# Performance work log

Measured on AMD Instinct MI355X. Metric: run time of the kernel, lower is better.

The kernel has to match this reference:

```python
import jax, jax.numpy as jnp
import numpy as np

DIM = 768
NUM_HEADS = 12
HEAD_DIM = DIM // NUM_HEADS
SCALE = HEAD_DIM ** -0.5


def setup_inputs() -> dict:
    key = jax.random.key(0)
    k1, k2, k3 = jax.random.split(key, 3)
    x = jax.random.normal(k1, (32, 577, DIM), dtype=jnp.float32)
    # torch nn.Linear weights are [out_features, in_features]
    W_qkv = jax.random.normal(k2, (3 * DIM, DIM), dtype=jnp.float32) * (DIM ** -0.5)
    W_proj = jax.random.normal(k3, (DIM, DIM), dtype=jnp.float32) * (DIM ** -0.5)
    b_proj = jnp.zeros((DIM,), dtype=jnp.float32)
    return {"x": x, "W_qkv": W_qkv, "W_proj": W_proj, "b_proj": b_proj}


def reference(x, W_qkv, W_proj, b_proj):
    B, N, C = x.shape
    H, D = NUM_HEADS, C // NUM_HEADS
    # qkv: [B, N, 3C] -> [3, B, H, N, D]
    qkv = (x @ W_qkv.T).reshape(B, N, 3, H, D).transpose(2, 0, 3, 1, 4)
    q, k, v = qkv[0], qkv[1], qkv[2]
    attn = jnp.einsum('bhnd,bhmd->bhnm', q, k) * SCALE
    attn = jax.nn.softmax(attn, axis=-1)
    out = jnp.einsum('bhnm,bhmd->bhnd', attn, v)  # [B, H, N, D]
    out = out.transpose(0, 2, 1, 3).reshape(B, N, C)
    return out @ W_proj.T + b_proj
```

## Files before the change

kernel.cpp:

```cpp
#include <hip/hip_runtime.h>
#include <math.h>

#define SEQ    577
#define BATCH  32
#define DIM    768
#define NHEAD  12
#define HDIM   64
#define MROWS  (BATCH * SEQ)
#define QKVN   (3 * DIM)

using half4   = __attribute__((ext_vector_type(4))) _Float16;
using half8   = __attribute__((ext_vector_type(8))) _Float16;
using floatx4 = __attribute__((ext_vector_type(4))) float;

typedef __attribute__((address_space(1))) const unsigned int GU;
typedef __attribute__((address_space(3))) unsigned int LU;

__device__ __forceinline__ void gld_lds16(const _Float16* g, _Float16* l) {
    __builtin_amdgcn_global_load_lds((const GU*)g, (LU*)l, 16, 0, 0);
}

__device__ __forceinline__ unsigned lds_addr(const void* p) {
    return (unsigned)(size_t)(LU*)p;
}

__global__ void cvt3_f32_f16(const float* __restrict__ a, _Float16* __restrict__ ao, int na4,
                             const float* __restrict__ b, _Float16* __restrict__ bo, int nb4,
                             const float* __restrict__ c, _Float16* __restrict__ co, int nc4)
{
    int i = blockIdx.x * blockDim.x + threadIdx.x;
    int stride = gridDim.x * blockDim.x;
    int total = na4 + nb4 + nc4;
    for (; i < total; i += stride) {
        const float4* src; half4* dst; int j = i;
        if (j < na4)            { src = (const float4*)a; dst = (half4*)ao; }
        else if ((j -= na4) < nb4) { src = (const float4*)b; dst = (half4*)bo; }
        else { j -= nb4;          src = (const float4*)c; dst = (half4*)co; }
        float4 v = src[j];
        half4 h;
        h[0] = (_Float16)v.x; h[1] = (_Float16)v.y;
        h[2] = (_Float16)v.z; h[3] = (_Float16)v.w;
        dst[j] = h;
    }
}

template<int OUT_HALF, int HAS_BIAS, int SCALEQ>
__global__ __launch_bounds__(256) void gemm_f16_lds(
    const _Float16* __restrict__ A, const _Float16* __restrict__ B,
    const float* __restrict__ bias, void* __restrict__ Cp,
    int M, int N, int K, int npm, int npn)
{
    __shared__ _Float16 As[2][128 * 32];
    __shared__ _Float16 Bs[2][128 * 32];

    const int GROUP = 8;
    int pid  = blockIdx.x;
    int ngrp = GROUP * npn;
    int g    = pid / ngrp;
    int fm   = g * GROUP;
    int gm   = npm - fm; if (gm > GROUP) gm = GROUP;
    int pm   = fm + (pid % ngrp) % gm;
    int pn   = (pid % ngrp) / gm;
    const int m0 = pm * 128, n0 = pn * 128;

    const int t    = threadIdx.x, lane = t & 63, wv = t >> 6;
    const int quad = lane >> 4,   ln   = lane & 15;
    const int wm   = wv >> 1,     wn   = wv & 1;

    floatx4 acc[4][4];
#pragma unroll
    for (int mt = 0; mt < 4; mt++)
#pragma unroll
        for (int nt = 0; nt < 4; nt++) acc[mt][nt] = {0.f, 0.f, 0.f, 0.f};

    const int sr  = wv * 32 + (lane >> 2);
    const int scl = (lane & 3) * 8;
    const int scg = ((lane & 3) ^ ((lane >> 3) & 3)) * 8;
    int ma0 = m0 + sr;      if (ma0 > M - 1) ma0 = M - 1;
    int ma1 = m0 + sr + 16; if (ma1 > M - 1) ma1 = M - 1;
    const _Float16* Ag0 = A + (size_t)ma0 * K + scg;
    const _Float16* Ag1 = A + (size_t)ma1 * K + scg;
    const _Float16* Bg0 = B + (size_t)(n0 + sr) * K + scg;
    const _Float16* Bg1 = B + (size_t)(n0 + sr + 16) * K + scg;
    const int l0 = sr * 32 + scl;
    const int l1 = (sr + 16) * 32 + scl;

    const int nk = K >> 5;

#define STAGE_G(it, buf)                                            \
    {                                                               \
        const int kn_ = (it) << 5;                                  \
        gld_lds16(Ag0 + kn_, &As[(buf)][l0]);                       \
        gld_lds16(Ag1 + kn_, &As[(buf)][l1]);                       \
        gld_lds16(Bg0 + kn_, &Bs[(buf)][l0]);                       \
        gld_lds16(Bg1 + kn_, &Bs[(buf)][l1]);                       \
    }

    STAGE_G(0, 0);
    STAGE_G(1, 1);

    const int rq = (ln >> 1) & 3;

    for (int it = 0; it < nk; it++) {
        const int cur = it & 1;

        if (it + 1 < nk) asm volatile("s_waitcnt vmcnt(4)" ::: "memory");
        else             asm volatile("s_waitcnt vmcnt(0)" ::: "memory");
        __builtin_amdgcn_s_barrier();
        __builtin_amdgcn_sched_barrier(0);

        half8 af[4], bf[4];
#pragma unroll
        for (int mt = 0; mt < 4; mt++)
            af[mt] = *(const half8*)&As[cur][(wm * 64 + mt * 16 + ln) * 32 + ((quad ^ rq) << 3)];
#pragma unroll
        for (int nt = 0; nt < 4; nt++)
            bf[nt] = *(const half8*)&Bs[cur][(wn * 64 + nt * 16 + ln) * 32 + ((quad ^ rq) << 3)];
#pragma unroll
        for (int mt = 0; mt < 4; mt++)
#pragma unroll
            for (int nt = 0; nt < 4; nt++)
                acc[mt][nt] = __builtin_amdgcn_mfma_f32_16x16x32_f16(
                    af[mt], bf[nt], acc[mt][nt], 0, 0, 0);

        __builtin_amdgcn_sched_barrier(0);
        __builtin_amdgcn_s_barrier();
        if (it + 2 < nk) STAGE_G(it + 2, cur);
    }
#undef STAGE_G

    float bv[4];
    if constexpr (HAS_BIAS) {
#pragma unroll
        for (int nt = 0; nt < 4; nt++) bv[nt] = bias[n0 + wn * 64 + nt * 16 + ln];
    }
    float*    C32 = (float*)Cp;
    _Float16* C16 = (_Float16*)Cp;
#pragma unroll
    for (int mt = 0; mt < 4; mt++)
#pragma unroll
        for (int r = 0; r < 4; r++) {
            int m = m0 + wm * 64 + mt * 16 + quad * 4 + r;
            if (m < M) {
#pragma unroll
                for (int nt = 0; nt < 4; nt++) {
                    int col = n0 + wn * 64 + nt * 16 + ln;
                    float v = acc[mt][nt][r];
                    if constexpr (HAS_BIAS) v += bv[nt];
                    if constexpr (SCALEQ) { if (col < DIM) v *= 0.18033688f; }
                    if constexpr (OUT_HALF) C16[(size_t)m * N + col] = (_Float16)v;
                    else                    C32[(size_t)m * N + col] = v;
                }
            }
        }
}

__global__ __launch_bounds__(256) void attn_f16(
    const _Float16* __restrict__ qkv, _Float16* __restrict__ outp)
{
    __shared__ _Float16 Ks[2][64 * 64];
    __shared__ _Float16 Vs[2][64 * 64];

    const int t    = threadIdx.x, lane = t & 63, wv = t >> 6;
    const int quad = lane >> 4,   ln   = lane & 15;
    const int q0   = blockIdx.x * 128;
    const int hd   = blockIdx.y,  b    = blockIdx.z;
    const _Float16* base = qkv + (size_t)b * SEQ * QKVN;

    half8 qreg[2][2];
#pragma unroll
    for (int qc = 0; qc < 2; qc++) {
        int q = q0 + wv * 32 + qc * 16 + ln; if (q >= SEQ) q = SEQ - 1;
#pragma unroll
        for (int kd = 0; kd < 2; kd++)
            qreg[qc][kd] = *(const half8*)(base + (size_t)q * QKVN + hd * HDIM + kd * 32 + quad * 8);
    }

    const int krow = t >> 3;
    const int kdc  = (t & 7) ^ (krow & 7);
    const int vkey = ((t >> 7) << 4) + (((t >> 3) & 3) << 2) + ((t >> 1) & 3);
    const int vd0  = (((t >> 5) & 3) << 4) + ((t & 1) << 3);
    const _Float16* kcst = base + DIM     + hd * HDIM + kdc * 8;
    const _Float16* vcst = base + 2 * DIM + hd * HDIM + vd0;

    float lr[2] = {0.f, 0.f};
    floatx4 o[2][4];
#pragma unroll
    for (int qc = 0; qc < 2; qc++)
#pragma unroll
        for (int dt = 0; dt < 4; dt++) o[qc][dt] = {0.f, 0.f, 0.f, 0.f};

    const unsigned vb0 = lds_addr(&Vs[0][0]) + lane * 8;

    gld_lds16(kcst + (size_t)krow * QKVN,        &Ks[0][t * 8]);
    gld_lds16(kcst + (size_t)(krow + 32) * QKVN, &Ks[0][(t + 256) * 8]);
    gld_lds16(vcst + (size_t)vkey * QKVN,        &Vs[0][t * 8]);
    gld_lds16(vcst + (size_t)(vkey + 32) * QKVN, &Vs[0][(t + 256) * 8]);

    for (int kt0 = 0; kt0 < 10; kt0++) {
        const int cur = kt0 & 1;
        const int k0  = kt0 * 64;

        __syncthreads();

        if (kt0 < 9) {
            const int k1 = k0 + 64, nb = cur ^ 1;
            int r0 = k1 + krow;      if (r0 > SEQ - 1) r0 = SEQ - 1;
            int r1 = k1 + krow + 32; if (r1 > SEQ - 1) r1 = SEQ - 1;
            int s0 = k1 + vkey;      if (s0 > SEQ - 1) s0 = SEQ - 1;
            int s1 = k1 + vkey + 32; if (s1 > SEQ - 1) s1 = SEQ - 1;
            gld_lds16(kcst + (size_t)r0 * QKVN, &Ks[nb][t * 8]);
            gld_lds16(kcst + (size_t)r1 * QKVN, &Ks[nb][(t + 256) * 8]);
            gld_lds16(vcst + (size_t)s0 * QKVN, &Vs[nb][t * 8]);
            gld_lds16(vcst + (size_t)s1 * QKVN, &Vs[nb][(t + 256) * 8]);
        }
        __builtin_amdgcn_sched_barrier(0);

        floatx4 sacc[2][4];
#pragma unroll
        for (int qc = 0; qc < 2; qc++)
#pragma unroll
            for (int mt = 0; mt < 4; mt++) sacc[qc][mt] = {0.f, 0.f, 0.f, 0.f};
        const int xr = ln & 7;
#pragma unroll
        for (int kd = 0; kd < 2; kd++) {
            half8 kf[4];
#pragma unroll
            for (int mt = 0; mt < 4; mt++)
                kf[mt] = *(const half8*)&Ks[cur][(mt * 16 + ln) * 64 + (((kd * 4 + quad) ^ xr) << 3)];
#pragma unroll
            for (int mt = 0; mt < 4; mt++) {
                sacc[0][mt] = __builtin_amdgcn_mfma_f32_16x16x32_f16(kf[mt], qreg[0][kd], sacc[0][mt], 0, 0, 0);
                sacc[1][mt] = __builtin_amdgcn_mfma_f32_16x16x32_f16(kf[mt], qreg[1][kd], sacc[1][mt], 0, 0, 0);
            }
        }

        half4 vf[4][4];
        const unsigned vb = vb0 + (cur << 13);
#pragma unroll
        for (int kt = 0; kt < 4; kt++) {
            unsigned a = vb + kt * 2048;
            asm volatile("ds_read_b64_tr_b16 %0, %1 offset:0"    : "=v"(vf[kt][0]) : "v"(a));
            asm volatile("ds_read_b64_tr_b16 %0, %1 offset:512"  : "=v"(vf[kt][1]) : "v"(a));
            asm volatile("ds_read_b64_tr_b16 %0, %1 offset:1024" : "=v"(vf[kt][2]) : "v"(a));
            asm volatile("ds_read_b64_tr_b16 %0, %1 offset:1536" : "=v"(vf[kt][3]) : "v"(a));
        }

        if (k0 + 64 > SEQ) {
#pragma unroll
            for (int mt = 0; mt < 4; mt++)
#pragma unroll
                for (int r = 0; r < 4; r++)
                    if (k0 + mt * 16 + quad * 4 + r >= SEQ) {
                        sacc[0][mt][r] = -3e38f;
                        sacc[1][mt][r] = -3e38f;
                    }
        }

        half4 pf[2][4];
#pragma unroll
        for (int qc = 0; qc < 2; qc++) {
#pragma unroll
            for (int mt = 0; mt < 4; mt++)
#pragma unroll
                for (int r = 0; r < 4; r++) {
                    float p = exp2f(sacc[qc][mt][r]);
                    lr[qc] += p;
                    pf[qc][mt][r] = (_Float16)p;
                }
        }

        asm volatile("s_waitcnt lgkmcnt(0)" ::: "memory");
        __builtin_amdgcn_sched_barrier(0);
#pragma unroll
        for (int kt = 0; kt < 4; kt++) {
#pragma unroll
            for (int dt = 0; dt < 4; dt++) {
                o[0][dt] = __builtin_amdgcn_mfma_f32_16x16x16f16(vf[kt][dt], pf[0][kt], o[0][dt], 0, 0, 0);
                o[1][dt] = __builtin_amdgcn_mfma_f32_16x16x16f16(vf[kt][dt], pf[1][kt], o[1][dt], 0, 0, 0);
            }
        }
    }

#pragma unroll
    for (int qc = 0; qc < 2; qc++) {
        lr[qc] += __shfl_xor(lr[qc], 16);
        lr[qc] += __shfl_xor(lr[qc], 32);
    }

#pragma unroll
    for (int qc = 0; qc < 2; qc++) {
        int q = q0 + wv * 32 + qc * 16 + ln;
        if (q < SEQ) {
            float inv = 1.f / lr[qc];
#pragma unroll
            for (int dt = 0; dt < 4; dt++) {
                half4 hv;
                hv[0] = (_Float16)(o[qc][dt][0] * inv);
                hv[1] = (_Float16)(o[qc][dt][1] * inv);
                hv[2] = (_Float16)(o[qc][dt][2] * inv);
                hv[3] = (_Float16)(o[qc][dt][3] * inv);
                *(half4*)&outp[(size_t)(b * SEQ + q) * DIM + hd * HDIM + dt * 16 + quad * 4] = hv;
            }
        }
    }
}

extern "C" void kernel_launch(void* const* d_in, const int* in_sizes, int n_in,
                              void* d_out, int out_size, void* d_ws, size_t ws_size,
                              hipStream_t stream)
{
    const float* x     = (const float*)d_in[0];
    const float* Wqkv  = (const float*)d_in[1];
    const float* Wproj = (const float*)d_in[2];
    const float* bproj = (const float*)d_in[3];
    float* out = (float*)d_out;

    const size_t NX  = (size_t)MROWS * DIM;
    const size_t NWQ = (size_t)QKVN * DIM;
    const size_t NWP = (size_t)DIM * DIM;

    _Float16* x16    = (_Float16*)d_ws;
    _Float16* Wq16   = x16 + NX;
    _Float16* Wp16   = Wq16 + NWQ;
    _Float16* qkv16  = Wp16 + NWP;
    _Float16* attn16 = qkv16 + (size_t)MROWS * QKVN;

    cvt3_f32_f16<<<2048, 256, 0, stream>>>(x, x16, (int)(NX / 4),
                                           Wqkv, Wq16, (int)(NWQ / 4),
                                           Wproj, Wp16, (int)(NWP / 4));

    {
        int npm = (MROWS + 127) / 128, npn = QKVN / 128;
        gemm_f16_lds<1, 0, 1><<<npm * npn, 256, 0, stream>>>(
            x16, Wq16, nullptr, qkv16, MROWS, QKVN, DIM, npm, npn);
    }

    attn_f16<<<dim3((SEQ + 127) / 128, NHEAD, BATCH), 256, 0, stream>>>(qkv16, attn16);

    {
        int npm = (MROWS + 127) / 128, npn = DIM / 128;
        gemm_f16_lds<0, 1, 0><<<npm * npn, 256, 0, stream>>>(
            attn16, Wp16, bproj, out, MROWS, DIM, DIM, npm, npn);
    }
}
```

Baseline: 339.3 us.

## Enlarge GEMM tiles to 256x256 with 512 threads and 64-deep K stages

Both projection GEMMs move from 128x128 tiles with 4 waves to 256x256 tiles with 8 waves, and each pipeline stage now covers 64 K elements split into two 32-wide LDS panels. Each wave computes a 128x64 sub-tile (8x4 MFMA tiles), so the ratio of MFMA work to LDS and global traffic rises and there are half as many K-loop barriers. The cost is 128 KB of LDS per block and a much larger accumulator register footprint. Grids also shrink sharply: the output projection gets only 73x3 blocks, which risks poor CU utilisation and a heavy partial last tile.

New measurement: 333.2 us. No clear change (-1.8%).

```diff
diff --git a/kernel.cpp b/kernel.cpp
--- a/kernel.cpp
+++ b/kernel.cpp
@@ -45,13 +45,13 @@
 }
 
 template<int OUT_HALF, int HAS_BIAS, int SCALEQ>
-__global__ __launch_bounds__(256) void gemm_f16_lds(
+__global__ __launch_bounds__(512, 2) void gemm_f16_256(
     const _Float16* __restrict__ A, const _Float16* __restrict__ B,
     const float* __restrict__ bias, void* __restrict__ Cp,
     int M, int N, int K, int npm, int npn)
 {
-    __shared__ _Float16 As[2][128 * 32];
-    __shared__ _Float16 Bs[2][128 * 32];
+    __shared__ _Float16 As[2][2 * 256 * 32];
+    __shared__ _Float16 Bs[2][2 * 256 * 32];
 
     const int GROUP = 8;
     int pid  = blockIdx.x;
@@ -61,39 +61,45 @@
     int gm   = npm - fm; if (gm > GROUP) gm = GROUP;
     int pm   = fm + (pid % ngrp) % gm;
     int pn   = (pid % ngrp) / gm;
-    const int m0 = pm * 128, n0 = pn * 128;
+    const int m0 = pm * 256, n0 = pn * 256;
 
     const int t    = threadIdx.x, lane = t & 63, wv = t >> 6;
     const int quad = lane >> 4,   ln   = lane & 15;
-    const int wm   = wv >> 1,     wn   = wv & 1;
-
-    floatx4 acc[4][4];
-#pragma unroll
-    for (int mt = 0; mt < 4; mt++)
+    const int wr   = wv >> 2,     wc   = wv & 3;
+
+    floatx4 acc[8][4];
+#pragma unroll
+    for (int mt = 0; mt < 8; mt++)
 #pragma unroll
         for (int nt = 0; nt < 4; nt++) acc[mt][nt] = {0.f, 0.f, 0.f, 0.f};
 
-    const int sr  = wv * 32 + (lane >> 2);
-    const int scl = (lane & 3) * 8;
-    const int scg = ((lane & 3) ^ ((lane >> 3) & 3)) * 8;
-    int ma0 = m0 + sr;      if (ma0 > M - 1) ma0 = M - 1;
-    int ma1 = m0 + sr + 16; if (ma1 > M - 1) ma1 = M - 1;
-    const _Float16* Ag0 = A + (size_t)ma0 * K + scg;
-    const _Float16* Ag1 = A + (size_t)ma1 * K + scg;
-    const _Float16* Bg0 = B + (size_t)(n0 + sr) * K + scg;
-    const _Float16* Bg1 = B + (size_t)(n0 + sr + 16) * K + scg;
-    const int l0 = sr * 32 + scl;
-    const int l1 = (sr + 16) * 32 + scl;
-
-    const int nk = K >> 5;
+    const _Float16* Ag[4];
+    const _Float16* Bg[4];
+    int ldst[4];
+#pragma unroll
+    for (int i = 0; i < 4; i++) {
+        const int CH    = t + (i << 9);
+        const int panel = CH >> 10;
+        const int rem   = CH & 1023;
+        const int row   = rem >> 2;
+        const int cc    = rem & 3;
+        const int scc   = cc ^ ((row >> 1) & 3);
+        int ma = m0 + row; if (ma > M - 1) ma = M - 1;
+        Ag[i]   = A + (size_t)ma * K + panel * 32 + scc * 8;
+        Bg[i]   = B + (size_t)(n0 + row) * K + panel * 32 + scc * 8;
+        ldst[i] = CH * 8;
+    }
+
+    const int nk = K >> 6;
 
 #define STAGE_G(it, buf)                                            \
     {                                                               \
-        const int kn_ = (it) << 5;                                  \
-        gld_lds16(Ag0 + kn_, &As[(buf)][l0]);                       \
-        gld_lds16(Ag1 + kn_, &As[(buf)][l1]);                       \
-        gld_lds16(Bg0 + kn_, &Bs[(buf)][l0]);                       \
-        gld_lds16(Bg1 + kn_, &Bs[(buf)][l1]);                       \
+        const int ko_ = (it) << 6;                                  \
+        _Pragma("unroll")                                           \
+        for (int i2 = 0; i2 < 4; i2++) {                            \
+            gld_lds16(Ag[i2] + ko_, &As[(buf)][ldst[i2]]);          \
+            gld_lds16(Bg[i2] + ko_, &Bs[(buf)][ldst[i2]]);          \
+        }                                                           \
     }
 
     STAGE_G(0, 0);
@@ -104,24 +110,27 @@
     for (int it = 0; it < nk; it++) {
         const int cur = it & 1;
 
-        if (it + 1 < nk) asm volatile("s_waitcnt vmcnt(4)" ::: "memory");
+        if (it + 1 < nk) asm volatile("s_waitcnt vmcnt(8)" ::: "memory");
         else             asm volatile("s_waitcnt vmcnt(0)" ::: "memory");
         __builtin_amdgcn_s_barrier();
         __builtin_amdgcn_sched_barrier(0);
 
-        half8 af[4], bf[4];
-#pragma unroll
-        for (int mt = 0; mt < 4; mt++)
-            af[mt] = *(const half8*)&As[cur][(wm * 64 + mt * 16 + ln) * 32 + ((quad ^ rq) << 3)];
-#pragma unroll
-        for (int nt = 0; nt < 4; nt++)
-            bf[nt] = *(const half8*)&Bs[cur][(wn * 64 + nt * 16 + ln) * 32 + ((quad ^ rq) << 3)];
-#pragma unroll
-        for (int mt = 0; mt < 4; mt++)
+#pragma unroll
+        for (int p = 0; p < 2; p++) {
+            half8 af[8], bf[4];
+#pragma unroll
+            for (int mt = 0; mt < 8; mt++)
+                af[mt] = *(const half8*)&As[cur][p * 8192 + (wr * 128 + mt * 16 + ln) * 32 + ((quad ^ rq) << 3)];
 #pragma unroll
             for (int nt = 0; nt < 4; nt++)
-                acc[mt][nt] = __builtin_amdgcn_mfma_f32_16x16x32_f16(
-                    af[mt], bf[nt], acc[mt][nt], 0, 0, 0);
+                bf[nt] = *(const half8*)&Bs[cur][p * 8192 + (wc * 64 + nt * 16 + ln) * 32 + ((quad ^ rq) << 3)];
+#pragma unroll
+            for (int mt = 0; mt < 8; mt++)
+#pragma unroll
+                for (int nt = 0; nt < 4; nt++)
+                    acc[mt][nt] = __builtin_amdgcn_mfma_f32_16x16x32_f16(
+                        af[mt], bf[nt], acc[mt][nt], 0, 0, 0);
+        }
 
         __builtin_amdgcn_sched_barrier(0);
         __builtin_amdgcn_s_barrier();
@@ -132,19 +141,19 @@
     float bv[4];
     if constexpr (HAS_BIAS) {
 #pragma unroll
-        for (int nt = 0; nt < 4; nt++) bv[nt] = bias[n0 + wn * 64 + nt * 16 + ln];
+        for (int nt = 0; nt < 4; nt++) bv[nt] = bias[n0 + wc * 64 + nt * 16 + ln];
     }
     float*    C32 = (float*)Cp;
     _Float16* C16 = (_Float16*)Cp;
 #pragma unroll
-    for (int mt = 0; mt < 4; mt++)
+    for (int mt = 0; mt < 8; mt++)
 #pragma unroll
         for (int r = 0; r < 4; r++) {
-            int m = m0 + wm * 64 + mt * 16 + quad * 4 + r;
+            int m = m0 + wr * 128 + mt * 16 + quad * 4 + r;
             if (m < M) {
 #pragma unroll
                 for (int nt = 0; nt < 4; nt++) {
-                    int col = n0 + wn * 64 + nt * 16 + ln;
+                    int col = n0 + wc * 64 + nt * 16 + ln;
                     float v = acc[mt][nt][r];
                     if constexpr (HAS_BIAS) v += bv[nt];
                     if constexpr (SCALEQ) { if (col < DIM) v *= 0.18033688f; }
@@ -331,16 +340,16 @@
                                            Wproj, Wp16, (int)(NWP / 4));
 
     {
-        int npm = (MROWS + 127) / 128, npn = QKVN / 128;
-        gemm_f16_lds<1, 0, 1><<<npm * npn, 256, 0, stream>>>(
+        int npm = (MROWS + 255) / 256, npn = QKVN / 256;
+        gemm_f16_256<1, 0, 1><<<npm * npn, 512, 0, stream>>>(
             x16, Wq16, nullptr, qkv16, MROWS, QKVN, DIM, npm, npn);
     }
 
     attn_f16<<<dim3((SEQ + 127) / 128, NHEAD, BATCH), 256, 0, stream>>>(qkv16, attn16);
 
     {
-        int npm = (MROWS + 127) / 128, npn = DIM / 128;
-        gemm_f16_lds<0, 1, 0><<<npm * npn, 256, 0, stream>>>(
+        int npm = (MROWS + 255) / 256, npn = DIM / 256;
+        gemm_f16_256<0, 1, 0><<<npm * npn, 512, 0, stream>>>(
             attn16, Wp16, bproj, out, MROWS, DIM, DIM, npm, npn);
     }
 }
```
